# Performance work log

Measured on AMD Instinct MI355X. Metric: run time of the kernel, lower is better.

## Reference

```python
import jax, jax.numpy as jnp
import numpy as np

EMBED_DIM = 1024
N_HEADS = 16
HEAD_DIM = EMBED_DIM // N_HEADS


def setup_inputs() -> dict:
    key = jax.random.key(0)
    k_x, k_wqkv, k_bqkv, k_wo, k_bo = jax.random.split(key, 5)
    s = 1.0 / np.sqrt(EMBED_DIM)
    return {
        "x": jax.random.normal(k_x, (2, 2048, EMBED_DIM), dtype=jnp.float32),
        "w_qkv": jax.random.uniform(k_wqkv, (EMBED_DIM, 3 * EMBED_DIM), jnp.float32, -s, s),
        "b_qkv": jax.random.uniform(k_bqkv, (3 * EMBED_DIM,), jnp.float32, -s, s),
        "w_out": jax.random.uniform(k_wo, (EMBED_DIM, EMBED_DIM), jnp.float32, -s, s),
        "b_out": jax.random.uniform(k_bo, (EMBED_DIM,), jnp.float32, -s, s),
    }


def reference(x, w_qkv, b_qkv, w_out, b_out):
    B, T, C = x.shape
    qkv = x @ w_qkv + b_qkv                      # [B,T,3C]
    q, k, v = jnp.split(qkv, 3, axis=-1)
    # [B,T,C] -> [B,H,T,D]
    def heads(t):
        return t.reshape(B, T, N_HEADS, HEAD_DIM).transpose(0, 2, 1, 3)
    q, k, v = heads(q), heads(k), heads(v)
    scale = 1.0 / np.sqrt(HEAD_DIM).astype(np.float32)
    scores = jnp.einsum("bhqd,bhkd->bhqk", q, k) * scale
    causal = jnp.tril(jnp.ones((T, T), dtype=bool))  # True where allowed
    scores = jnp.where(causal, scores, jnp.finfo(scores.dtype).min)
    attn = jax.nn.softmax(scores, axis=-1)
    out = jnp.einsum("bhqk,bhkd->bhqd", attn, v)
    out = out.transpose(0, 2, 1, 3).reshape(B, T, C)
    return out @ w_out + b_out
```

## Files before the change

### kernel.cpp

```cpp
#include <hip/hip_runtime.h>
#include <hip/hip_bf16.h>

typedef __attribute__((ext_vector_type(4))) float f32x4;
typedef __attribute__((ext_vector_type(8))) short bf16x8;

static __device__ __forceinline__ unsigned short f2bf(float f) {
  union { float f; unsigned u; } v;
  v.f = f;
  unsigned r = v.u + 0x7FFFu + ((v.u >> 16) & 1u);
  return (unsigned short)(r >> 16);
}

static __device__ __forceinline__ void gload16(const void* g, void* lds) {
  __builtin_amdgcn_global_load_lds(
      (const __attribute__((address_space(1))) unsigned int*)g,
      (__attribute__((address_space(3))) unsigned int*)lds, 16, 0, 0);
}

__global__ __launch_bounds__(256) void cast_bf16_kernel(
    const float* __restrict__ in, unsigned short* __restrict__ out) {
  int i = blockIdx.x * 256 + threadIdx.x;
  float4 v = reinterpret_cast<const float4*>(in)[i];
  ushort4 o;
  o.x = f2bf(v.x); o.y = f2bf(v.y); o.z = f2bf(v.z); o.w = f2bf(v.w);
  reinterpret_cast<ushort4*>(out)[i] = o;
}

__global__ __launch_bounds__(256) void transpose_cast_kernel(
    const float* __restrict__ in, unsigned short* __restrict__ out, int R, int C) {
  __shared__ float tile[32][33];
  int c0 = blockIdx.x * 32, r0 = blockIdx.y * 32;
  int tx = threadIdx.x & 31, ty = threadIdx.x >> 5;
#pragma unroll
  for (int i = 0; i < 32; i += 8)
    tile[ty + i][tx] = in[(size_t)(r0 + ty + i) * C + c0 + tx];
  __syncthreads();
#pragma unroll
  for (int i = 0; i < 32; i += 8)
    out[(size_t)(c0 + ty + i) * R + r0 + tx] = f2bf(tile[tx][ty + i]);
}

template <int MODE>
__global__ __launch_bounds__(256) void gemm_bf16(
    const unsigned short* __restrict__ A,
    const unsigned short* __restrict__ Bt,
    const float* __restrict__ bias,
    unsigned short* __restrict__ q_out,
    unsigned short* __restrict__ k_out,
    unsigned short* __restrict__ v_out,
    float* __restrict__ f_out) {
  __shared__ __align__(16) unsigned short As[128 * 32];
  __shared__ __align__(16) unsigned short Bs[128 * 32];

  const int tid = threadIdx.x;
  const int wid = tid >> 6, lane = tid & 63;
  const int l15 = lane & 15, g = lane >> 4;
  const int wm = wid >> 1, wn = wid & 1;
  const int n0 = blockIdx.x * 128, m0 = blockIdx.y * 128;

  f32x4 acc[4][4] = {};

  for (int k0 = 0; k0 < 1024; k0 += 32) {
    __syncthreads();
#pragma unroll
    for (int i = 0; i < 2; ++i) {
      int t = tid + i * 256;
      int row = t >> 2;
      int c8 = (t & 3) << 3;
      gload16(A + (size_t)(m0 + row) * 1024 + k0 + c8, As + (i * 256 + wid * 64) * 8);
      gload16(Bt + (size_t)(n0 + row) * 1024 + k0 + c8, Bs + (i * 256 + wid * 64) * 8);
    }
    __syncthreads();
    bf16x8 a[4], b[4];
#pragma unroll
    for (int mi = 0; mi < 4; ++mi)
      a[mi] = *reinterpret_cast<const bf16x8*>(As + (wm * 64 + mi * 16 + l15) * 32 + g * 8);
#pragma unroll
    for (int ni = 0; ni < 4; ++ni)
      b[ni] = *reinterpret_cast<const bf16x8*>(Bs + (wn * 64 + ni * 16 + l15) * 32 + g * 8);
#pragma unroll
    for (int mi = 0; mi < 4; ++mi)
#pragma unroll
      for (int ni = 0; ni < 4; ++ni)
        acc[mi][ni] = __builtin_amdgcn_mfma_f32_16x16x32_bf16(a[mi], b[ni], acc[mi][ni], 0, 0, 0);
  }

  if (MODE == 0) {
    const int which = n0 >> 10;
    unsigned short* dst = (which == 0) ? q_out : (which == 1) ? k_out : v_out;
#pragma unroll
    for (int ni = 0; ni < 4; ++ni) {
      int col = n0 + wn * 64 + ni * 16 + l15;
      int c = col & 1023;
      int h = c >> 6, d = c & 63;
      float bv = bias[col];
#pragma unroll
      for (int mi = 0; mi < 4; ++mi) {
#pragma unroll
        for (int r = 0; r < 4; ++r) {
          int rowg = m0 + wm * 64 + mi * 16 + g * 4 + r;
          int bb = rowg >> 11, tt = rowg & 2047;
          dst[((bb * 16 + h) * 2048 + tt) * 64 + d] = f2bf(acc[mi][ni][r] + bv);
        }
      }
    }
  } else {
#pragma unroll
    for (int ni = 0; ni < 4; ++ni) {
      int col = n0 + wn * 64 + ni * 16 + l15;
      float bv = bias[col];
#pragma unroll
      for (int mi = 0; mi < 4; ++mi)
#pragma unroll
        for (int r = 0; r < 4; ++r) {
          int rowg = m0 + wm * 64 + mi * 16 + g * 4 + r;
          f_out[(size_t)rowg * 1024 + col] = acc[mi][ni][r] + bv;
        }
    }
  }
}

#define KS_SZ (64 * 64)
#define VT_SZ (64 * 72)

__device__ __forceinline__ void attn_stage_K(const unsigned short* __restrict__ Kb,
                                             int k0, unsigned short* KsBuf,
                                             int tid, int wid) {
#pragma unroll
  for (int i = 0; i < 2; ++i) {
    int t = tid + i * 256;
    int row = t >> 3;
    int cb = (t & 7) << 4;
    int src = cb ^ ((row & 7) << 4);
    gload16((const char*)Kb + (size_t)(k0 + row) * 128 + src,
            (char*)KsBuf + (i * 256 + wid * 64) * 16);
  }
}

__device__ __forceinline__ void write_vt(unsigned short* VtBuf, int kvL, int d8,
                                         bf16x8 va, bf16x8 vb) {
#pragma unroll
  for (int j = 0; j < 8; ++j) {
    unsigned pk = (unsigned)(unsigned short)va[j] |
                  ((unsigned)(unsigned short)vb[j] << 16);
    *reinterpret_cast<unsigned*>(&VtBuf[(d8 + j) * 72 + kvL]) = pk;
  }
}

__device__ __forceinline__ void attn_run_qtile(
    const unsigned short* __restrict__ Qb,
    const unsigned short* __restrict__ Kb,
    const unsigned short* __restrict__ Vb,
    unsigned short* __restrict__ O,
    int b, int h, int q0, int nt,
    unsigned short* Ks, unsigned short* Vt, unsigned short* Ps,
    int tid, int wid, int l15, int g) {
  const float SC = 0.125f * 1.44269504f;

  bf16x8 qf[2];
  {
    const unsigned short* qrow = Qb + (size_t)(q0 + wid * 16 + l15) * 64;
    qf[0] = *reinterpret_cast<const bf16x8*>(qrow + g * 8);
    qf[1] = *reinterpret_cast<const bf16x8*>(qrow + 32 + g * 8);
  }

  float m_run = -1e30f, l_run = 0.0f;
  f32x4 ot[4] = {};
  const int qg = q0 + wid * 16 + l15;
  const int kvL = (tid & 31) * 2, d8 = (tid >> 5) * 8;

  attn_stage_K(Kb, 0, Ks, tid, wid);
  {
    const unsigned short* vp = Vb + (size_t)kvL * 64 + d8;
    bf16x8 va = *reinterpret_cast<const bf16x8*>(vp);
    bf16x8 vb = *reinterpret_cast<const bf16x8*>(vp + 64);
    write_vt(Vt, kvL, d8, va, vb);
  }
  __syncthreads();

  for (int t = 0; t < nt; ++t) {
    const unsigned short* KsC = Ks + (t & 1) * KS_SZ;
    const unsigned short* VtC = Vt + (t & 1) * VT_SZ;
    bf16x8 va, vb;
    const bool pf = (t + 1 < nt);
    if (pf) {
      attn_stage_K(Kb, (t + 1) << 6, Ks + ((t + 1) & 1) * KS_SZ, tid, wid);
      const unsigned short* vp = Vb + (size_t)(((t + 1) << 6) + kvL) * 64 + d8;
      va = *reinterpret_cast<const bf16x8*>(vp);
      vb = *reinterpret_cast<const bf16x8*>(vp + 64);
    }

    f32x4 s[4] = {};
    __builtin_amdgcn_s_setprio(1);
#pragma unroll
    for (int kk = 0; kk < 2; ++kk)
#pragma unroll
      for (int mi = 0; mi < 4; ++mi) {
        int row = mi * 16 + l15;
        int cb = (kk * 64 + g * 16) ^ ((row & 7) << 4);
        bf16x8 kf = *reinterpret_cast<const bf16x8*>((const char*)KsC + row * 128 + cb);
        s[mi] = __builtin_amdgcn_mfma_f32_16x16x32_bf16(kf, qf[kk], s[mi], 0, 0, 0);
      }
    __builtin_amdgcn_s_setprio(0);

    float tmax = -1e30f;
    if (t == nt - 1) {
      const int k0 = t << 6;
#pragma unroll
      for (int mi = 0; mi < 4; ++mi)
#pragma unroll
        for (int r = 0; r < 4; ++r) {
          int kvg = k0 + mi * 16 + g * 4 + r;
          float sv = s[mi][r] * SC;
          sv = (kvg <= qg) ? sv : -1e30f;
          s[mi][r] = sv;
          tmax = fmaxf(tmax, sv);
        }
    } else {
#pragma unroll
      for (int mi = 0; mi < 4; ++mi)
#pragma unroll
        for (int r = 0; r < 4; ++r) {
          float sv = s[mi][r] * SC;
          s[mi][r] = sv;
          tmax = fmaxf(tmax, sv);
        }
    }
    tmax = fmaxf(tmax, __shfl_xor(tmax, 16));
    tmax = fmaxf(tmax, __shfl_xor(tmax, 32));

    if (!__all(tmax <= m_run + 8.0f)) {
      float m_new = fmaxf(m_run, tmax);
      float corr = __builtin_amdgcn_exp2f(m_run - m_new);
      l_run *= corr;
#pragma unroll
      for (int mi = 0; mi < 4; ++mi)
#pragma unroll
        for (int r = 0; r < 4; ++r) ot[mi][r] *= corr;
      m_run = m_new;
    }

    float tsum = 0.f;
    const int qrow = wid * 16 + l15;
#pragma unroll
    for (int mi = 0; mi < 4; ++mi) {
#pragma unroll
      for (int r2 = 0; r2 < 2; ++r2) {
        float p0 = __builtin_amdgcn_exp2f(s[mi][2 * r2] - m_run);
        float p1 = __builtin_amdgcn_exp2f(s[mi][2 * r2 + 1] - m_run);
        tsum += p0 + p1;
        unsigned pk = (unsigned)f2bf(p0) | ((unsigned)f2bf(p1) << 16);
        *reinterpret_cast<unsigned*>(&Ps[qrow * 72 + mi * 16 + g * 4 + 2 * r2]) = pk;
      }
    }
    tsum += __shfl_xor(tsum, 16);
    tsum += __shfl_xor(tsum, 32);
    l_run += tsum;

    __builtin_amdgcn_s_setprio(1);
#pragma unroll
    for (int kk = 0; kk < 2; ++kk) {
      bf16x8 pfr = *reinterpret_cast<const bf16x8*>(Ps + qrow * 72 + kk * 32 + g * 8);
#pragma unroll
      for (int mi = 0; mi < 4; ++mi) {
        bf16x8 vf = *reinterpret_cast<const bf16x8*>(VtC + (mi * 16 + l15) * 72 + kk * 32 + g * 8);
        ot[mi] = __builtin_amdgcn_mfma_f32_16x16x32_bf16(vf, pfr, ot[mi], 0, 0, 0);
      }
    }
    __builtin_amdgcn_s_setprio(0);

    if (pf) write_vt(Vt + ((t + 1) & 1) * VT_SZ, kvL, d8, va, vb);
    __syncthreads();
  }

  float inv_l = 1.0f / l_run;
#pragma unroll
  for (int mi = 0; mi < 4; ++mi)
#pragma unroll
    for (int r = 0; r < 4; ++r) {
      int q = wid * 16 + l15;
      int d = mi * 16 + g * 4 + r;
      int cb = (d * 2) ^ ((q & 7) << 4);
      *reinterpret_cast<unsigned short*>((char*)Ks + q * 128 + cb) = f2bf(ot[mi][r] * inv_l);
    }
  __syncthreads();
#pragma unroll
  for (int i = 0; i < 2; ++i) {
    int t = tid + i * 256;
    int row = t >> 3;
    int cb = (t & 7) << 4;
    int sw = cb ^ ((row & 7) << 4);
    bf16x8 vv = *reinterpret_cast<const bf16x8*>((const char*)Ks + row * 128 + sw);
    *reinterpret_cast<bf16x8*>(O + ((size_t)(b * 2048 + q0 + row)) * 1024 + h * 64 + (cb >> 1)) = vv;
  }
  __syncthreads();
}

__global__ __launch_bounds__(256) void attn_fwd(
    const unsigned short* __restrict__ Q,
    const unsigned short* __restrict__ K,
    const unsigned short* __restrict__ V,
    unsigned short* __restrict__ O) {
  __shared__ __align__(16) unsigned short Ks[2 * KS_SZ];
  __shared__ __align__(16) unsigned short Vt[2 * VT_SZ];
  __shared__ __align__(16) unsigned short Ps[64 * 72];

  const int tid = threadIdx.x;
  const int wid = tid >> 6;
  const int l15 = tid & 15;
  const int g = (tid & 63) >> 4;

  int lin = blockIdx.x + (blockIdx.y << 4);
  int w = ((lin & 7) << 6) + (lin >> 3);
  const int pi = w & 15, bh = w >> 4;
  const int b = bh >> 4, h = bh & 15;

  const unsigned short* Qb = Q + (size_t)bh * 2048 * 64;
  const unsigned short* Kb = K + (size_t)bh * 2048 * 64;
  const unsigned short* Vb = V + (size_t)bh * 2048 * 64;

  attn_run_qtile(Qb, Kb, Vb, O, b, h, pi << 6, pi + 1, Ks, Vt, Ps, tid, wid, l15, g);
  attn_run_qtile(Qb, Kb, Vb, O, b, h, (31 - pi) << 6, 32 - pi, Ks, Vt, Ps, tid, wid, l15, g);
}

extern "C" void kernel_launch(void* const* d_in, const int* in_sizes, int n_in,
                              void* d_out, int out_size, void* d_ws, size_t ws_size,
                              hipStream_t stream) {
  const float* x = (const float*)d_in[0];
  const float* w_qkv = (const float*)d_in[1];
  const float* b_qkv = (const float*)d_in[2];
  const float* w_out = (const float*)d_in[3];
  const float* b_out = (const float*)d_in[4];
  float* out = (float*)d_out;
  char* ws = (char*)d_ws;

  unsigned short* xb    = (unsigned short*)d_out;
  unsigned short* wqkvT = (unsigned short*)(ws);
  unsigned short* woT   = (unsigned short*)(ws + 6291456);
  unsigned short* q_buf = (unsigned short*)(ws + 8388608);
  unsigned short* k_buf = (unsigned short*)(ws + 16777216);
  unsigned short* v_buf = (unsigned short*)(ws + 25165824);
  unsigned short* aout  = (unsigned short*)(ws + 33554432);

  cast_bf16_kernel<<<dim3(4096), dim3(256), 0, stream>>>(x, xb);
  transpose_cast_kernel<<<dim3(96, 32), dim3(256), 0, stream>>>(w_qkv, wqkvT, 1024, 3072);
  transpose_cast_kernel<<<dim3(32, 32), dim3(256), 0, stream>>>(w_out, woT, 1024, 1024);

  gemm_bf16<0><<<dim3(24, 32), dim3(256), 0, stream>>>(
      xb, wqkvT, b_qkv, q_buf, k_buf, v_buf, nullptr);

  attn_fwd<<<dim3(16, 32), dim3(256), 0, stream>>>(q_buf, k_buf, v_buf, aout);

  gemm_bf16<1><<<dim3(8, 32), dim3(256), 0, stream>>>(
      aout, woT, b_out, nullptr, nullptr, nullptr, out);
}
```

Measured before the change: 123.8 us.

## Load K fragments directly into registers with prefetch instead of LDS staging

Removes the double-buffered LDS staging of K tiles in the attention kernel. Each wave now loads its K MFMA fragments straight from global memory into registers, prefetching the next tile into a second register set and swapping at the end of the iteration. The row-max reduction becomes a tree instead of a serial chain, and the output scratch now reuses the Vt buffer. This cuts LDS traffic and shared memory use, which may raise occupancy. In exchange, each of the 4 waves re-reads the full K tile from global/L2 instead of sharing one copy, and the extra register arrays add register pressure.

```diff
diff --git a/kernel.cpp b/kernel.cpp
--- a/kernel.cpp
+++ b/kernel.cpp
@@ -120,22 +120,7 @@
   }
 }
 
-#define KS_SZ (64 * 64)
 #define VT_SZ (64 * 72)
-
-__device__ __forceinline__ void attn_stage_K(const unsigned short* __restrict__ Kb,
-                                             int k0, unsigned short* KsBuf,
-                                             int tid, int wid) {
-#pragma unroll
-  for (int i = 0; i < 2; ++i) {
-    int t = tid + i * 256;
-    int row = t >> 3;
-    int cb = (t & 7) << 4;
-    int src = cb ^ ((row & 7) << 4);
-    gload16((const char*)Kb + (size_t)(k0 + row) * 128 + src,
-            (char*)KsBuf + (i * 256 + wid * 64) * 16);
-  }
-}
 
 __device__ __forceinline__ void write_vt(unsigned short* VtBuf, int kvL, int d8,
                                          bf16x8 va, bf16x8 vb) {
@@ -153,7 +138,7 @@
     const unsigned short* __restrict__ Vb,
     unsigned short* __restrict__ O,
     int b, int h, int q0, int nt,
-    unsigned short* Ks, unsigned short* Vt, unsigned short* Ps,
+    unsigned short* Vt, unsigned short* Ps,
     int tid, int wid, int l15, int g) {
   const float SC = 0.125f * 1.44269504f;
 
@@ -164,12 +149,21 @@
     qf[1] = *reinterpret_cast<const bf16x8*>(qrow + 32 + g * 8);
   }
 
+  const unsigned short* Kl = Kb + (size_t)l15 * 64 + g * 8;
+
   float m_run = -1e30f, l_run = 0.0f;
   f32x4 ot[4] = {};
   const int qg = q0 + wid * 16 + l15;
   const int kvL = (tid & 31) * 2, d8 = (tid >> 5) * 8;
-
-  attn_stage_K(Kb, 0, Ks, tid, wid);
+  const int qrow = wid * 16 + l15;
+
+  bf16x8 kc[2][4], kn[2][4];
+
+#pragma unroll
+  for (int kk = 0; kk < 2; ++kk)
+#pragma unroll
+    for (int mi = 0; mi < 4; ++mi)
+      kc[kk][mi] = *reinterpret_cast<const bf16x8*>(Kl + (size_t)(mi * 16) * 64 + kk * 32);
   {
     const unsigned short* vp = Vb + (size_t)kvL * 64 + d8;
     bf16x8 va = *reinterpret_cast<const bf16x8*>(vp);
@@ -179,15 +173,19 @@
   __syncthreads();
 
   for (int t = 0; t < nt; ++t) {
-    const unsigned short* KsC = Ks + (t & 1) * KS_SZ;
     const unsigned short* VtC = Vt + (t & 1) * VT_SZ;
     bf16x8 va, vb;
     const bool pf = (t + 1 < nt);
     if (pf) {
-      attn_stage_K(Kb, (t + 1) << 6, Ks + ((t + 1) & 1) * KS_SZ, tid, wid);
       const unsigned short* vp = Vb + (size_t)(((t + 1) << 6) + kvL) * 64 + d8;
       va = *reinterpret_cast<const bf16x8*>(vp);
       vb = *reinterpret_cast<const bf16x8*>(vp + 64);
+      const unsigned short* kp = Kl + ((size_t)(t + 1) << 12);
+#pragma unroll
+      for (int kk = 0; kk < 2; ++kk)
+#pragma unroll
+        for (int mi = 0; mi < 4; ++mi)
+          kn[kk][mi] = *reinterpret_cast<const bf16x8*>(kp + (size_t)(mi * 16) * 64 + kk * 32);
     }
 
     f32x4 s[4] = {};
@@ -195,15 +193,10 @@
 #pragma unroll
     for (int kk = 0; kk < 2; ++kk)
 #pragma unroll
-      for (int mi = 0; mi < 4; ++mi) {
-        int row = mi * 16 + l15;
-        int cb = (kk * 64 + g * 16) ^ ((row & 7) << 4);
-        bf16x8 kf = *reinterpret_cast<const bf16x8*>((const char*)KsC + row * 128 + cb);
-        s[mi] = __builtin_amdgcn_mfma_f32_16x16x32_bf16(kf, qf[kk], s[mi], 0, 0, 0);
-      }
+      for (int mi = 0; mi < 4; ++mi)
+        s[mi] = __builtin_amdgcn_mfma_f32_16x16x32_bf16(kc[kk][mi], qf[kk], s[mi], 0, 0, 0);
     __builtin_amdgcn_s_setprio(0);
 
-    float tmax = -1e30f;
     if (t == nt - 1) {
       const int k0 = t << 6;
 #pragma unroll
@@ -212,20 +205,19 @@
         for (int r = 0; r < 4; ++r) {
           int kvg = k0 + mi * 16 + g * 4 + r;
           float sv = s[mi][r] * SC;
-          sv = (kvg <= qg) ? sv : -1e30f;
-          s[mi][r] = sv;
-          tmax = fmaxf(tmax, sv);
+          s[mi][r] = (kvg <= qg) ? sv : -1e30f;
         }
     } else {
 #pragma unroll
       for (int mi = 0; mi < 4; ++mi)
 #pragma unroll
-        for (int r = 0; r < 4; ++r) {
-          float sv = s[mi][r] * SC;
-          s[mi][r] = sv;
-          tmax = fmaxf(tmax, sv);
-        }
-    }
+        for (int r = 0; r < 4; ++r) s[mi][r] *= SC;
+    }
+    float mx[4];
+#pragma unroll
+    for (int mi = 0; mi < 4; ++mi)
+      mx[mi] = fmaxf(fmaxf(s[mi][0], s[mi][1]), fmaxf(s[mi][2], s[mi][3]));
+    float tmax = fmaxf(fmaxf(mx[0], mx[1]), fmaxf(mx[2], mx[3]));
     tmax = fmaxf(tmax, __shfl_xor(tmax, 16));
     tmax = fmaxf(tmax, __shfl_xor(tmax, 32));
 
@@ -241,7 +233,6 @@
     }
 
     float tsum = 0.f;
-    const int qrow = wid * 16 + l15;
 #pragma unroll
     for (int mi = 0; mi < 4; ++mi) {
 #pragma unroll
@@ -269,19 +260,26 @@
     }
     __builtin_amdgcn_s_setprio(0);
 
-    if (pf) write_vt(Vt + ((t + 1) & 1) * VT_SZ, kvL, d8, va, vb);
+    if (pf) {
+      write_vt(Vt + ((t + 1) & 1) * VT_SZ, kvL, d8, va, vb);
+#pragma unroll
+      for (int kk = 0; kk < 2; ++kk)
+#pragma unroll
+        for (int mi = 0; mi < 4; ++mi) kc[kk][mi] = kn[kk][mi];
+    }
     __syncthreads();
   }
 
+  unsigned short* scr = Vt;
   float inv_l = 1.0f / l_run;
 #pragma unroll
   for (int mi = 0; mi < 4; ++mi)
 #pragma unroll
     for (int r = 0; r < 4; ++r) {
-      int q = wid * 16 + l15;
       int d = mi * 16 + g * 4 + r;
-      int cb = (d * 2) ^ ((q & 7) << 4);
-      *reinterpret_cast<unsigned short*>((char*)Ks + q * 128 + cb) = f2bf(ot[mi][r] * inv_l);
+      int cb = (d * 2) ^ ((qrow & 7) << 4);
+      *reinterpret_cast<unsigned short*>((char*)scr + qrow * 128 + cb) =
+          f2bf(ot[mi][r] * inv_l);
     }
   __syncthreads();
 #pragma unroll
@@ -290,7 +288,7 @@
     int row = t >> 3;
     int cb = (t & 7) << 4;
     int sw = cb ^ ((row & 7) << 4);
-    bf16x8 vv = *reinterpret_cast<const bf16x8*>((const char*)Ks + row * 128 + sw);
+    bf16x8 vv = *reinterpret_cast<const bf16x8*>((const char*)scr + row * 128 + sw);
     *reinterpret_cast<bf16x8*>(O + ((size_t)(b * 2048 + q0 + row)) * 1024 + h * 64 + (cb >> 1)) = vv;
   }
   __syncthreads();
@@ -301,7 +299,6 @@
     const unsigned short* __restrict__ K,
     const unsigned short* __restrict__ V,
     unsigned short* __restrict__ O) {
-  __shared__ __align__(16) unsigned short Ks[2 * KS_SZ];
   __shared__ __align__(16) unsigned short Vt[2 * VT_SZ];
   __shared__ __align__(16) unsigned short Ps[64 * 72];
 
@@ -319,8 +316,8 @@
   const unsigned short* Kb = K + (size_t)bh * 2048 * 64;
   const unsigned short* Vb = V + (size_t)bh * 2048 * 64;
 
-  attn_run_qtile(Qb, Kb, Vb, O, b, h, pi << 6, pi + 1, Ks, Vt, Ps, tid, wid, l15, g);
-  attn_run_qtile(Qb, Kb, Vb, O, b, h, (31 - pi) << 6, 32 - pi, Ks, Vt, Ps, tid, wid, l15, g);
+  attn_run_qtile(Qb, Kb, Vb, O, b, h, pi << 6, pi + 1, Vt, Ps, tid, wid, l15, g);
+  attn_run_qtile(Qb, Kb, Vb, O, b, h, (31 - pi) << 6, 32 - pi, Vt, Ps, tid, wid, l15, g);
 }
 
 extern "C" void kernel_launch(void* const* d_in, const int* in_sizes, int n_in,
```

Measured after the change: 149.5 us. +20.8%, slower.
